# Kernel optimization log

Measured on AMD Instinct MI355X. Metric: run time of the kernel, lower is better.

Reference implementation:

```python
import jax, jax.numpy as jnp
import numpy as np

WIN = (4, 4, 4)   # (wd, wh, ww), window seq len s = 64
HEADS = 4


def setup_inputs() -> dict:
    key = jax.random.key(0)
    k1, k2, k3 = jax.random.split(key, 3)
    B, D, H, W, C = 1, 32, 64, 128, 96
    x = jax.random.normal(k1, (B, D, H, W, C), dtype=jnp.float32)
    # weights stored in (in, out) layout; math identical to torch Linear (x @ W.T)
    w_qkv = jax.random.normal(k2, (C, 3 * C), dtype=jnp.float32) * (C ** -0.5)
    w_proj = jax.random.normal(k3, (C, C), dtype=jnp.float32) * (C ** -0.5)
    b_proj = jnp.zeros((C,), dtype=jnp.float32)
    return {"x": x, "w_qkv": w_qkv, "w_proj": w_proj, "b_proj": b_proj}


def reference(x, w_qkv, w_proj, b_proj):
    B, D, H, W, C = x.shape
    wd, wh, ww = WIN
    h = HEADS
    ch = C // h
    s = wd * wh * ww
    scale = ch ** -0.5
    n, m, l = D // wd, H // wh, W // ww
    # window partition: [B,D,H,W,C] -> [B,n,m,l,s,C]
    xw = x.reshape(B, n, wd, m, wh, l, ww, C)
    xw = xw.transpose(0, 1, 3, 5, 2, 4, 6, 7).reshape(B, n, m, l, s, C)
    # QKV projection (no bias)
    qkv = xw @ w_qkv                      # [B,n,m,l,s,3C]
    q, k, v = jnp.split(qkv, 3, axis=-1)  # each [B,n,m,l,s,C]

    def to_heads(t):
        return t.reshape(B, n, m, l, s, h, ch).transpose(0, 1, 2, 3, 5, 4, 6)

    q, k, v = to_heads(q), to_heads(k), to_heads(v)  # [B,n,m,l,h,s,ch]
    attn = jnp.einsum('bnmlhsc,bnmlhtc->bnmlhst', q, k) * scale
    attn = jax.nn.softmax(attn, axis=-1)             # [B,n,m,l,h,s,s]
    out = jnp.einsum('bnmlhst,bnmlhtc->bnmlhsc', attn, v)
    # merge heads: [B,n,m,l,h,s,ch] -> [B,n,m,l,s,C]
    out = out.transpose(0, 1, 2, 3, 5, 4, 6).reshape(B, n, m, l, s, C)
    out = out @ w_proj + b_proj
    # window merge back to [B,D,H,W,C]
    out = out.reshape(B, n, m, l, wd, wh, ww, C)
    out = out.transpose(0, 1, 4, 2, 5, 3, 6, 7).reshape(B, D, H, W, C)
    return out
```

## Files before the change

### kernel.cpp

```cpp
#include <hip/hip_runtime.h>
#include <hip/hip_bf16.h>

typedef __attribute__((ext_vector_type(8))) short bf16x8;
typedef __attribute__((ext_vector_type(4))) float f32x4;
typedef __attribute__((ext_vector_type(4))) unsigned short u16x4;
typedef __attribute__((ext_vector_type(4))) unsigned int u32x4;
typedef __attribute__((ext_vector_type(2))) unsigned int u32x2;

#define MFMA16(a, b, c) __builtin_amdgcn_mfma_f32_16x16x32_bf16((a), (b), (c), 0, 0, 0)

#define WQT_ELEMS 27648
#define WPT_ELEMS 9216

__device__ __forceinline__ unsigned short cvt_bf(float f) {
    __hip_bfloat16 h = __float2bfloat16(f);
    return *reinterpret_cast<unsigned short*>(&h);
}
__device__ __forceinline__ unsigned pack2bf(float a, float b) {
    return (unsigned)cvt_bf(a) | ((unsigned)cvt_bf(b) << 16);
}

__global__ void wconv_kernel(const float* __restrict__ wqkv,
                             const float* __restrict__ wproj,
                             unsigned short* __restrict__ wsT) {
    int o = blockIdx.x * 256 + threadIdx.x;
    if (o < WQT_ELEMS) {
        int j = o / 96, c = o % 96;
        float w = wqkv[c * 288 + j];
        if (j < 96) w *= 0.2944889313f;
        wsT[o] = cvt_bf(w);
    } else if (o < WQT_ELEMS + WPT_ELEMS) {
        int o2 = o - WQT_ELEMS;
        int j = o2 / 96, c = o2 % 96;
        wsT[o] = cvt_bf(wproj[c * 96 + j]);
    }
}

__device__ __forceinline__ int xq_addr(int t, int c) {
    return ((c >> 5) << 12) + ((t >> 1) << 7)
         + ((((t & 1) << 6) + ((c & 31) << 1)) ^ (((t >> 1) & 7) << 4));
}

#define LOADW(m, W0, W1, W2) do {                                              \
    const unsigned short* _wp = wsT + ((m) * 16 + p) * 96 + qg * 8;            \
    W0 = *reinterpret_cast<const bf16x8*>(_wp);                                \
    W1 = *reinterpret_cast<const bf16x8*>(_wp + 32);                           \
    W2 = *reinterpret_cast<const bf16x8*>(_wp + 64);                           \
} while (0)

#define MFMA_T(W0, W1, W2)                                                     \
    f32x4 ac0 = fzero, ac1 = fzero, ac2 = fzero, ac3 = fzero;                  \
    __builtin_amdgcn_s_setprio(1);                                             \
    ac0 = MFMA16(W0, a00, ac0); ac1 = MFMA16(W0, a10, ac1);                    \
    ac2 = MFMA16(W0, a20, ac2); ac3 = MFMA16(W0, a30, ac3);                    \
    ac0 = MFMA16(W1, a01, ac0); ac1 = MFMA16(W1, a11, ac1);                    \
    ac2 = MFMA16(W1, a21, ac2); ac3 = MFMA16(W1, a31, ac3);                    \
    ac0 = MFMA16(W2, a02, ac0); ac1 = MFMA16(W2, a12, ac1);                    \
    ac2 = MFMA16(W2, a22, ac2); ac3 = MFMA16(W2, a32, ac3);                    \
    __builtin_amdgcn_s_setprio(0);

#define DO_QK(DST, ch, W0, W1, W2) do {                                        \
    MFMA_T(W0, W1, W2)                                                         \
    char* _d = (DST) + xq_addr(p, (ch));                                       \
    *reinterpret_cast<u32x2*>(_d)        = (u32x2){pack2bf(ac0[0],ac0[1]), pack2bf(ac0[2],ac0[3])}; \
    *reinterpret_cast<u32x2*>(_d + 1024) = (u32x2){pack2bf(ac1[0],ac1[1]), pack2bf(ac1[2],ac1[3])}; \
    *reinterpret_cast<u32x2*>(_d + 2048) = (u32x2){pack2bf(ac2[0],ac2[1]), pack2bf(ac2[2],ac2[3])}; \
    *reinterpret_cast<u32x2*>(_d + 3072) = (u32x2){pack2bf(ac3[0],ac3[1]), pack2bf(ac3[2],ac3[3])}; \
} while (0)

#define DO_Q(m, W0, W1, W2) DO_QK(qb, (m) * 16 + 4 * qg, W0, W1, W2)
#define DO_K(m, W0, W1, W2) DO_QK(kb, ((m) - 6) * 16 + 4 * qg, W0, W1, W2)

#define STV1(JV, A, T2) do {                                                   \
    int _r0 = (JV);                                                            \
    *reinterpret_cast<unsigned short*>(vtb + (_r0)     * 128 + ((T2) ^ (((_r0)     & 7) << 4))) = cvt_bf(A[0]); \
    *reinterpret_cast<unsigned short*>(vtb + (_r0 + 1) * 128 + ((T2) ^ (((_r0 + 1) & 7) << 4))) = cvt_bf(A[1]); \
    *reinterpret_cast<unsigned short*>(vtb + (_r0 + 2) * 128 + ((T2) ^ (((_r0 + 2) & 7) << 4))) = cvt_bf(A[2]); \
    *reinterpret_cast<unsigned short*>(vtb + (_r0 + 3) * 128 + ((T2) ^ (((_r0 + 3) & 7) << 4))) = cvt_bf(A[3]); \
} while (0)

#define DO_V(m, W0, W1, W2) do {                                               \
    MFMA_T(W0, W1, W2)                                                         \
    int jv = ((m) - 12) * 16 + 4 * qg;                                         \
    STV1(jv, ac0, (p) * 2);                                                    \
    STV1(jv, ac1, (16 + p) * 2);                                               \
    STV1(jv, ac2, (32 + p) * 2);                                               \
    STV1(jv, ac3, (48 + p) * 2);                                               \
} while (0)

#define LOADWP(m, W0, W1, W2) do {                                             \
    const unsigned short* _wp = wpT + ((m) * 16 + p) * 96 + qg * 8;            \
    W0 = *reinterpret_cast<const bf16x8*>(_wp);                                \
    W1 = *reinterpret_cast<const bf16x8*>(_wp + 32);                           \
    W2 = *reinterpret_cast<const bf16x8*>(_wp + 64);                           \
} while (0)

#define PROJ(m, W0, W1, W2) do {                                               \
    f32x4 acc = fzero;                                                         \
    __builtin_amdgcn_s_setprio(1);                                             \
    acc = MFMA16(W0, o0, acc);                                                 \
    acc = MFMA16(W1, o1, acc);                                                 \
    acc = MFMA16(W2, o2, acc);                                                 \
    __builtin_amdgcn_s_setprio(0);                                             \
    float4 bb = *reinterpret_cast<const float4*>(bproj + (m) * 16 + 4 * qg);   \
    f32x4 r;                                                                   \
    r[0] = acc[0] + bb.x; r[1] = acc[1] + bb.y;                                \
    r[2] = acc[2] + bb.z; r[3] = acc[3] + bb.w;                                \
    *reinterpret_cast<f32x4*>(out + obase + (m) * 16 + 4 * qg) = r;            \
} while (0)

__global__ __launch_bounds__(256, 3)
void winattn_kernel(const float* __restrict__ x,
                    const unsigned short* __restrict__ wsT,
                    const float* __restrict__ bproj,
                    float* __restrict__ out) {
    __shared__ __align__(16) char LDS[50176];
    char* const qb  = LDS;
    char* const xq  = LDS + 12288;
    char* const kb  = LDS + 24576;
    char* const vtb = LDS + 36864;

    const int tid = threadIdx.x;
    const int lane = tid & 63;
    const int wv = tid >> 6;
    const int p  = lane & 15;
    const int qg = lane >> 4;

    const int iw  = blockIdx.x;
    const int l_i = iw & 31;
    const int m_i = (iw >> 5) & 15;
    const int n_i = iw >> 9;

    const f32x4 fzero = {0.f, 0.f, 0.f, 0.f};
    const bf16x8 zero8 = {0, 0, 0, 0, 0, 0, 0, 0};

    bf16x8 wA0, wA1, wA2, wB0, wB1, wB2;
    const int tb0 = (wv < 3) ? wv * 4 : 15;
    LOADW(tb0, wA0, wA1, wA2);

    {
        int t = tid / 24, cq = tid - t * 24;
        #pragma unroll
        for (int it = 0; it < 6; ++it) {
            int td = t >> 4, th = (t >> 2) & 3, tw = t & 3;
            int off = (((n_i * 4 + td) * 64 + (m_i * 4 + th)) * 128 + (l_i * 4 + tw)) * 96 + cq * 4;
            float4 v4 = *reinterpret_cast<const float4*>(x + off);
            u16x4 h;
            h[0] = cvt_bf(v4.x); h[1] = cvt_bf(v4.y); h[2] = cvt_bf(v4.z); h[3] = cvt_bf(v4.w);
            *reinterpret_cast<u16x4*>(xq + xq_addr(t, cq * 4)) = h;
            cq += 16;
            int carry = (cq >= 24) ? 1 : 0;
            cq -= carry ? 24 : 0;
            t += 10 + carry;
        }
    }
    __syncthreads();

    bf16x8 a00, a01, a02, a10, a11, a12, a20, a21, a22, a30, a31, a32;
    {
        const char* xb0 = xq + xq_addr(p, qg * 8);
        const char* xb1 = xq + xq_addr(p, 32 + qg * 8);
        const char* xb2 = xq + xq_addr(p, 64 + qg * 8);
        a00 = *reinterpret_cast<const bf16x8*>(xb0);
        a01 = *reinterpret_cast<const bf16x8*>(xb1);
        a02 = *reinterpret_cast<const bf16x8*>(xb2);
        a10 = *reinterpret_cast<const bf16x8*>(xb0 + 1024);
        a11 = *reinterpret_cast<const bf16x8*>(xb1 + 1024);
        a12 = *reinterpret_cast<const bf16x8*>(xb2 + 1024);
        a20 = *reinterpret_cast<const bf16x8*>(xb0 + 2048);
        a21 = *reinterpret_cast<const bf16x8*>(xb1 + 2048);
        a22 = *reinterpret_cast<const bf16x8*>(xb2 + 2048);
        a30 = *reinterpret_cast<const bf16x8*>(xb0 + 3072);
        a31 = *reinterpret_cast<const bf16x8*>(xb1 + 3072);
        a32 = *reinterpret_cast<const bf16x8*>(xb2 + 3072);
    }

    if (wv == 0) {
        LOADW(1,  wB0, wB1, wB2); DO_Q(0,  wA0, wA1, wA2);
        LOADW(2,  wA0, wA1, wA2); DO_Q(1,  wB0, wB1, wB2);
        LOADW(3,  wB0, wB1, wB2); DO_Q(2,  wA0, wA1, wA2);
        LOADW(12, wA0, wA1, wA2); DO_Q(3,  wB0, wB1, wB2);
        DO_V(12, wA0, wA1, wA2);
    } else if (wv == 1) {
        LOADW(5,  wB0, wB1, wB2); DO_Q(4,  wA0, wA1, wA2);
        LOADW(6,  wA0, wA1, wA2); DO_Q(5,  wB0, wB1, wB2);
        LOADW(7,  wB0, wB1, wB2); DO_K(6,  wA0, wA1, wA2);
        LOADW(13, wA0, wA1, wA2); DO_K(7,  wB0, wB1, wB2);
        DO_V(13, wA0, wA1, wA2);
    } else if (wv == 2) {
        LOADW(9,  wB0, wB1, wB2); DO_K(8,  wA0, wA1, wA2);
        LOADW(10, wA0, wA1, wA2); DO_K(9,  wB0, wB1, wB2);
        LOADW(11, wB0, wB1, wB2); DO_K(10, wA0, wA1, wA2);
        LOADW(14, wA0, wA1, wA2); DO_K(11, wB0, wB1, wB2);
        DO_V(14, wA0, wA1, wA2);
    } else {
        LOADW(16, wB0, wB1, wB2); DO_V(15, wA0, wA1, wA2);
        LOADW(17, wA0, wA1, wA2); DO_V(16, wB0, wB1, wB2);
        DO_V(17, wA0, wA1, wA2);
    }
    __syncthreads();

    const unsigned short* wpT = wsT + WQT_ELEMS;
    bf16x8 wp0, wp1, wp2;
    LOADWP(0, wp0, wp1, wp2);

    #pragma unroll 2
    for (int hd = 0; hd < 4; ++hd) {
        int qc = hd * 24 + qg * 8;
        bf16x8 aq_raw = *reinterpret_cast<const bf16x8*>(qb + xq_addr(wv * 16 + p, qc));
        bf16x8 aqh = (qg == 3) ? zero8 : aq_raw;
        const char* akb = kb + xq_addr(p, qc);
        f32x4 sacc[4];
        __builtin_amdgcn_s_setprio(1);
        sacc[0] = MFMA16(*reinterpret_cast<const bf16x8*>(akb),        aqh, fzero);
        sacc[1] = MFMA16(*reinterpret_cast<const bf16x8*>(akb + 1024), aqh, fzero);
        sacc[2] = MFMA16(*reinterpret_cast<const bf16x8*>(akb + 2048), aqh, fzero);
        sacc[3] = MFMA16(*reinterpret_cast<const bf16x8*>(akb + 3072), aqh, fzero);
        __builtin_amdgcn_s_setprio(0);
        float sum = 0.f;
        unsigned pk[4][2];
        #pragma unroll
        for (int nt = 0; nt < 4; ++nt) {
            float e0 = exp2f(sacc[nt][0]);
            float e1 = exp2f(sacc[nt][1]);
            float e2 = exp2f(sacc[nt][2]);
            float e3 = exp2f(sacc[nt][3]);
            sum += (e0 + e1) + (e2 + e3);
            pk[nt][0] = pack2bf(e0, e1);
            pk[nt][1] = pack2bf(e2, e3);
        }
        u32x4 pa0, pa1;
        #pragma unroll
        for (int d = 0; d < 4; ++d) {
            int src = ((qg & 1) * 2 + (d >> 1)) * 16 + p;
            int lo0 = __shfl((int)pk[0][d & 1], src);
            int hi0 = __shfl((int)pk[1][d & 1], src);
            int lo1 = __shfl((int)pk[2][d & 1], src);
            int hi1 = __shfl((int)pk[3][d & 1], src);
            pa0[d] = (qg < 2) ? (unsigned)lo0 : (unsigned)hi0;
            pa1[d] = (qg < 2) ? (unsigned)lo1 : (unsigned)hi1;
        }
        bf16x8 pA0 = __builtin_bit_cast(bf16x8, pa0);
        bf16x8 pA1 = __builtin_bit_cast(bf16x8, pa1);
        sum += __shfl_xor(sum, 16);
        sum += __shfl_xor(sum, 32);
        float inv = 1.0f / sum;
        f32x4 oacc[2] = {fzero, fzero};
        __builtin_amdgcn_s_setprio(1);
        #pragma unroll
        for (int n2 = 0; n2 < 2; ++n2) {
            int vr = hd * 24 + n2 * 16 + p;
            int rb = vr * 128, sw = (vr & 7) << 4;
            bf16x8 av0 = *reinterpret_cast<const bf16x8*>(vtb + rb + ((qg * 16) ^ sw));
            bf16x8 av1 = *reinterpret_cast<const bf16x8*>(vtb + rb + ((64 + qg * 16) ^ sw));
            oacc[n2] = MFMA16(av0, pA0, oacc[n2]);
            oacc[n2] = MFMA16(av1, pA1, oacc[n2]);
        }
        __builtin_amdgcn_s_setprio(0);
        {
            u32x2 w0 = { pack2bf(oacc[0][0] * inv, oacc[0][1] * inv),
                         pack2bf(oacc[0][2] * inv, oacc[0][3] * inv) };
            *reinterpret_cast<u32x2*>(xq + xq_addr(wv * 16 + p, hd * 24 + 4 * qg)) = w0;
            if (qg < 2) {
                u32x2 w1 = { pack2bf(oacc[1][0] * inv, oacc[1][1] * inv),
                             pack2bf(oacc[1][2] * inv, oacc[1][3] * inv) };
                *reinterpret_cast<u32x2*>(xq + xq_addr(wv * 16 + p, hd * 24 + 16 + 4 * qg)) = w1;
            }
        }
    }

    bf16x8 o0, o1, o2;
    o0 = *reinterpret_cast<const bf16x8*>(xq + xq_addr(wv * 16 + p, qg * 8));
    o1 = *reinterpret_cast<const bf16x8*>(xq + xq_addr(wv * 16 + p, 32 + qg * 8));
    o2 = *reinterpret_cast<const bf16x8*>(xq + xq_addr(wv * 16 + p, 64 + qg * 8));

    const int obase = (((n_i * 4 + wv) * 64 + (m_i * 4 + (p >> 2))) * 128
                       + (l_i * 4 + (p & 3))) * 96;
    LOADWP(1, wB0, wB1, wB2); PROJ(0, wp0, wp1, wp2);
    LOADWP(2, wA0, wA1, wA2); PROJ(1, wB0, wB1, wB2);
    LOADWP(3, wB0, wB1, wB2); PROJ(2, wA0, wA1, wA2);
    LOADWP(4, wA0, wA1, wA2); PROJ(3, wB0, wB1, wB2);
    LOADWP(5, wB0, wB1, wB2); PROJ(4, wA0, wA1, wA2);
    PROJ(5, wB0, wB1, wB2);
}

extern "C" void kernel_launch(void* const* d_in, const int* in_sizes, int n_in,
                              void* d_out, int out_size, void* d_ws, size_t ws_size,
                              hipStream_t stream) {
    const float* x     = (const float*)d_in[0];
    const float* wqkv  = (const float*)d_in[1];
    const float* wproj = (const float*)d_in[2];
    const float* bproj = (const float*)d_in[3];
    float* out = (float*)d_out;
    unsigned short* wsT = (unsigned short*)d_ws;

    wconv_kernel<<<dim3((WQT_ELEMS + WPT_ELEMS) / 256), dim3(256), 0, stream>>>(wqkv, wproj, wsT);
    winattn_kernel<<<dim3(4096), dim3(256), 0, stream>>>(x, wsT, bproj, out);
}
```

Before: 74.75 us.

## Load x fragments straight from global memory, drop LDS staging buffer

```diff
diff --git a/kernel.cpp b/kernel.cpp
--- a/kernel.cpp
+++ b/kernel.cpp
@@ -48,6 +48,15 @@
     W2 = *reinterpret_cast<const bf16x8*>(_wp + 64);                           \
 } while (0)
 
+#define LDFRAG(FR, NTOFF, KT) do {                                             \
+    f32x4 _lo = *reinterpret_cast<const f32x4*>(xtok + (NTOFF) + (KT) * 32);   \
+    f32x4 _hi = *reinterpret_cast<const f32x4*>(xtok + (NTOFF) + (KT) * 32 + 4); \
+    u32x4 _w;                                                                  \
+    _w[0] = pack2bf(_lo[0], _lo[1]); _w[1] = pack2bf(_lo[2], _lo[3]);          \
+    _w[2] = pack2bf(_hi[0], _hi[1]); _w[3] = pack2bf(_hi[2], _hi[3]);          \
+    FR = __builtin_bit_cast(bf16x8, _w);                                       \
+} while (0)
+
 #define MFMA_T(W0, W1, W2)                                                     \
     f32x4 ac0 = fzero, ac1 = fzero, ac2 = fzero, ac3 = fzero;                  \
     __builtin_amdgcn_s_setprio(1);                                             \
@@ -114,11 +123,10 @@
                     const unsigned short* __restrict__ wsT,
                     const float* __restrict__ bproj,
                     float* __restrict__ out) {
-    __shared__ __align__(16) char LDS[50176];
+    __shared__ __align__(16) char LDS[37888];
     char* const qb  = LDS;
-    char* const xq  = LDS + 12288;
-    char* const kb  = LDS + 24576;
-    char* const vtb = LDS + 36864;
+    char* const kb  = LDS + 12288;
+    char* const vtb = LDS + 24576;
 
     const int tid = threadIdx.x;
     const int lane = tid & 63;
@@ -138,42 +146,13 @@
     const int tb0 = (wv < 3) ? wv * 4 : 15;
     LOADW(tb0, wA0, wA1, wA2);
 
-    {
-        int t = tid / 24, cq = tid - t * 24;
-        #pragma unroll
-        for (int it = 0; it < 6; ++it) {
-            int td = t >> 4, th = (t >> 2) & 3, tw = t & 3;
-            int off = (((n_i * 4 + td) * 64 + (m_i * 4 + th)) * 128 + (l_i * 4 + tw)) * 96 + cq * 4;
-            float4 v4 = *reinterpret_cast<const float4*>(x + off);
-            u16x4 h;
-            h[0] = cvt_bf(v4.x); h[1] = cvt_bf(v4.y); h[2] = cvt_bf(v4.z); h[3] = cvt_bf(v4.w);
-            *reinterpret_cast<u16x4*>(xq + xq_addr(t, cq * 4)) = h;
-            cq += 16;
-            int carry = (cq >= 24) ? 1 : 0;
-            cq -= carry ? 24 : 0;
-            t += 10 + carry;
-        }
-    }
-    __syncthreads();
-
+    const float* xtok = x + (((n_i * 4) * 64 + m_i * 4 + (p >> 2)) * 128
+                             + l_i * 4 + (p & 3)) * 96 + qg * 8;
     bf16x8 a00, a01, a02, a10, a11, a12, a20, a21, a22, a30, a31, a32;
-    {
-        const char* xb0 = xq + xq_addr(p, qg * 8);
-        const char* xb1 = xq + xq_addr(p, 32 + qg * 8);
-        const char* xb2 = xq + xq_addr(p, 64 + qg * 8);
-        a00 = *reinterpret_cast<const bf16x8*>(xb0);
-        a01 = *reinterpret_cast<const bf16x8*>(xb1);
-        a02 = *reinterpret_cast<const bf16x8*>(xb2);
-        a10 = *reinterpret_cast<const bf16x8*>(xb0 + 1024);
-        a11 = *reinterpret_cast<const bf16x8*>(xb1 + 1024);
-        a12 = *reinterpret_cast<const bf16x8*>(xb2 + 1024);
-        a20 = *reinterpret_cast<const bf16x8*>(xb0 + 2048);
-        a21 = *reinterpret_cast<const bf16x8*>(xb1 + 2048);
-        a22 = *reinterpret_cast<const bf16x8*>(xb2 + 2048);
-        a30 = *reinterpret_cast<const bf16x8*>(xb0 + 3072);
-        a31 = *reinterpret_cast<const bf16x8*>(xb1 + 3072);
-        a32 = *reinterpret_cast<const bf16x8*>(xb2 + 3072);
-    }
+    LDFRAG(a00, 0,       0); LDFRAG(a01, 0,       1); LDFRAG(a02, 0,       2);
+    LDFRAG(a10, 786432,  0); LDFRAG(a11, 786432,  1); LDFRAG(a12, 786432,  2);
+    LDFRAG(a20, 1572864, 0); LDFRAG(a21, 1572864, 1); LDFRAG(a22, 1572864, 2);
+    LDFRAG(a30, 2359296, 0); LDFRAG(a31, 2359296, 1); LDFRAG(a32, 2359296, 2);
 
     if (wv == 0) {
         LOADW(1,  wB0, wB1, wB2); DO_Q(0,  wA0, wA1, wA2);
@@ -260,19 +239,19 @@
         {
             u32x2 w0 = { pack2bf(oacc[0][0] * inv, oacc[0][1] * inv),
                          pack2bf(oacc[0][2] * inv, oacc[0][3] * inv) };
-            *reinterpret_cast<u32x2*>(xq + xq_addr(wv * 16 + p, hd * 24 + 4 * qg)) = w0;
+            *reinterpret_cast<u32x2*>(qb + xq_addr(wv * 16 + p, hd * 24 + 4 * qg)) = w0;
             if (qg < 2) {
                 u32x2 w1 = { pack2bf(oacc[1][0] * inv, oacc[1][1] * inv),
                              pack2bf(oacc[1][2] * inv, oacc[1][3] * inv) };
-                *reinterpret_cast<u32x2*>(xq + xq_addr(wv * 16 + p, hd * 24 + 16 + 4 * qg)) = w1;
+                *reinterpret_cast<u32x2*>(qb + xq_addr(wv * 16 + p, hd * 24 + 16 + 4 * qg)) = w1;
             }
         }
     }
 
     bf16x8 o0, o1, o2;
-    o0 = *reinterpret_cast<const bf16x8*>(xq + xq_addr(wv * 16 + p, qg * 8));
-    o1 = *reinterpret_cast<const bf16x8*>(xq + xq_addr(wv * 16 + p, 32 + qg * 8));
-    o2 = *reinterpret_cast<const bf16x8*>(xq + xq_addr(wv * 16 + p, 64 + qg * 8));
+    o0 = *reinterpret_cast<const bf16x8*>(qb + xq_addr(wv * 16 + p, qg * 8));
+    o1 = *reinterpret_cast<const bf16x8*>(qb + xq_addr(wv * 16 + p, 32 + qg * 8));
+    o2 = *reinterpret_cast<const bf16x8*>(qb + xq_addr(wv * 16 + p, 64 + qg * 8));
 
     const int obase = (((n_i * 4 + wv) * 64 + (m_i * 4 + (p >> 2))) * 128
                        + (l_i * 4 + (p & 3))) * 96;
```

New measurement: 94.11 us. 1.26x slower.
